# Optimization experiments

Measured on AMD Instinct MI355X. Metric: run time of the kernel, lower is better.

Reference implementation:

```python
import jax, jax.numpy as jnp
import numpy as np

B, SE, HD, ED, N, T = 64, 512, 1024, 512, 10000, 20
EOS_ID = 1
NEG_BIG = -1e9    # stand-in for -MAX_VAL encoder pad mask
MASK_VAL = -1e7   # logits_mask scatter value (-10000000.0 in torch)
M = HD + ED


def setup_inputs() -> dict:
    key = jax.random.key(0)
    ks = jax.random.split(key, 16)
    s = 0.02
    enc = jax.random.normal(ks[0], (B, SE, HD), jnp.float32)
    hidden = jax.random.normal(ks[1], (1, B, HD), jnp.float32)
    cell = jax.random.normal(ks[2], (1, B, HD), jnp.float32)
    text_lengths = jax.random.randint(ks[3], (B,), SE // 2, SE + 1)
    encoder_mask = jnp.arange(SE)[None, :] < text_lengths[:, None]  # [B,SE] bool
    embedding = jax.random.normal(ks[4], (N, ED), jnp.float32) * s
    # LSTM (PyTorch gate order i,f,g,o)
    w_ih = jax.random.normal(ks[5], (4 * HD, ED), jnp.float32) * s
    w_hh = jax.random.normal(ks[6], (4 * HD, HD), jnp.float32) * s
    b_ih = jnp.zeros((4 * HD,), jnp.float32)
    b_hh = jnp.zeros((4 * HD,), jnp.float32)
    # dense_net: Hd -> He
    w_q = jax.random.normal(ks[7], (HD, HD), jnp.float32) * s
    b_q = jnp.zeros((HD,), jnp.float32)
    # SelfAttentiveSum: Linear(Ed,Ed)+ReLU+Linear(Ed,1)
    w_k = jax.random.normal(ks[8], (ED, ED), jnp.float32) * s
    b_k = jnp.zeros((ED,), jnp.float32)
    w_ko = jax.random.normal(ks[9], (ED,), jnp.float32) * s
    b_ko = jnp.zeros((), jnp.float32)
    # MLP: Linear(M,M)+ReLU+Linear(M,N)
    w_m1 = jax.random.normal(ks[10], (M, M), jnp.float32) * s
    b_m1 = jnp.zeros((M,), jnp.float32)
    w_m2 = jax.random.normal(ks[11], (N, M), jnp.float32) * s
    b_m2 = jnp.zeros((N,), jnp.float32)
    return dict(encoded_hidden_embeddings=enc, hidden=hidden, cell=cell,
                text_lengths=text_lengths, encoder_mask=encoder_mask,
                embedding=embedding, w_ih=w_ih, w_hh=w_hh, b_ih=b_ih, b_hh=b_hh,
                w_q=w_q, b_q=b_q, w_k=w_k, b_k=b_k, w_ko=w_ko, b_ko=b_ko,
                w_m1=w_m1, b_m1=b_m1, w_m2=w_m2, b_m2=b_m2)


def _decode(enc, h0, c0, encoder_mask, embedding, w_ih, w_hh, b_ih, b_hh,
            w_q, b_q, w_k, b_k, w_ko, b_ko, w_m1, b_m1, w_m2, b_m2):
    pad_mask = jnp.where(encoder_mask, 0.0, NEG_BIG).astype(enc.dtype)  # [B,SE]
    sent = enc[:, 0, :]  # [B,HD] sentence representation (dropout is identity in eval)

    def step(carry, t):
        h, c, inp, logits_mask, buf = carry
        # --- LSTM cell (single step) ---
        gates = inp @ w_ih.T + b_ih + h @ w_hh.T + b_hh  # [B,4HD]
        i, f, g, o = jnp.split(gates, 4, axis=-1)
        c = jax.nn.sigmoid(f) * c + jax.nn.sigmoid(i) * jnp.tanh(g)
        h = jax.nn.sigmoid(o) * jnp.tanh(c)
        # --- attention over encoder states ---
        q = h @ w_q.T + b_q                                   # [B,HD]
        score = jnp.einsum('bsh,bh->bs', enc, q) + pad_mask    # [B,SE]
        w = jax.nn.softmax(score, axis=1)
        attn_enc = jnp.einsum('bs,bsh->bh', w, enc)            # [B,HD]
        # --- self-attentive sum over previously predicted label embeddings ---
        valid = jnp.arange(T) < jnp.maximum(t, 1)              # step 0: zeros row 0 valid
        k = jax.nn.relu(buf @ w_k.T + b_k) @ w_ko + b_ko       # [B,T]
        k = jnp.where(valid[None, :], k, NEG_BIG)
        sw = jax.nn.softmax(k, axis=1)
        attn_last = jnp.einsum('bt,bte->be', sw, buf)          # [B,ED]
        # --- MLP ---
        m = jnp.concatenate([sent + attn_enc, inp + attn_last], axis=-1)  # [B,M]
        logits = jax.nn.relu(m @ w_m1.T + b_m1) @ w_m2.T + b_m2 + logits_mask  # [B,N]
        next_ids = jnp.argmax(logits, axis=-1)                 # [B]
        pred_emb = embedding[next_ids]                          # [B,ED]
        buf = buf.at[:, t].set(pred_emb)
        logits_mask = logits_mask.at[jnp.arange(B), next_ids].set(MASK_VAL)
        logits_mask = logits_mask.at[:, EOS_ID].set(0.0)
        return (h, c, pred_emb, logits_mask, buf), (logits, next_ids)

    init = (h0, c0,
            jnp.zeros((B, ED), enc.dtype),
            jnp.zeros((B, N), enc.dtype),
            jnp.zeros((B, T, ED), enc.dtype))
    _, (outs, ids) = jax.lax.scan(step, init, jnp.arange(T))
    return jnp.transpose(outs, (1, 0, 2)), jnp.transpose(ids, (1, 0))  # [B,T,N],[B,T]


def reference(encoded_hidden_embeddings, hidden, cell, text_lengths, encoder_mask,
              embedding, w_ih, w_hh, b_ih, b_hh, w_q, b_q, w_k, b_k, w_ko, b_ko,
              w_m1, b_m1, w_m2, b_m2):
    # De=1: [1,B,HD] -> [B,HD]
    return _decode(encoded_hidden_embeddings, hidden[0], cell[0], encoder_mask,
                   embedding, w_ih, w_hh, b_ih, b_hh, w_q, b_q, w_k, b_k,
                   w_ko, b_ko, w_m1, b_m1, w_m2, b_m2)
```

## Files before the change

kernel.cpp:

```cpp
#include <hip/hip_runtime.h>

#define B64 64
#define SE 512
#define HD 1024
#define ED 512
#define NV 10000
#define TT 20
#define MM 1536
#define MASK_VALF -10000000.0f

#define OFF_XT    0
#define OFF_CT    98304
#define OFF_A     163840
#define OFF_B     4003840
#define OFF_QF    5052416
#define OFF_FM    5117952
#define OFF_FL    5118976
#define OFF_XT2   5120000
#define OFF_H1T   5218304
#define OFF_ARGV  5316608
#define OFF_ARGI  5396608
#define OFF_MASKT 5476608
#define OFF_BUF   6116608
#define OFF_BUFT  6771968
#define OFF_KVP   7427328

__device__ __forceinline__ float sigmoidf_(float x) { return 1.f / (1.f + expf(-x)); }

__global__ __launch_bounds__(256) void k_init(const float* __restrict__ h0,
                                              const float* __restrict__ c0,
                                              float* __restrict__ ws) {
  int idx = blockIdx.x * 256 + threadIdx.x, stride = gridDim.x * 256;
  float* inpT = ws + OFF_XT;
  float* hT = ws + OFF_XT + 512 * 64;
  float* cT = ws + OFF_CT;
  float* maskT = ws + OFF_MASKT;
  float* buf = ws + OFF_BUF;
  float* bufT = ws + OFF_BUFT;
  for (int i = idx; i < 512 * 64; i += stride) inpT[i] = 0.f;
  for (int i = idx; i < NV * 64; i += stride) maskT[i] = 0.f;
  for (int i = idx; i < B64 * TT * ED; i += stride) { buf[i] = 0.f; bufT[i] = 0.f; }
  for (int i = idx; i < HD * 64; i += stride) {
    int u = i >> 6, b = i & 63;
    hT[i] = h0[b * HD + u];
    cT[i] = c0[b * HD + u];
  }
}

template <int KT>
__global__ __launch_bounds__(256) void k_gemm(const float* __restrict__ W, int ldW,
                                              const float* __restrict__ x,
                                              float* __restrict__ part, int nrows, size_t psz) {
  __shared__ float wl[32][KT];
  int tid = threadIdx.x;
  int r0b = blockIdx.x * 32;
  int split = blockIdx.y;
  int k0 = split * KT;
  constexpr int NF4 = 32 * KT / 4;
  for (int i = tid; i < NF4; i += 256) {
    int r = i / (KT / 4), kk = (i % (KT / 4)) * 4;
    int gr = r0b + r;
    if (gr > nrows - 1) gr = nrows - 1;
    *(float4*)&wl[r][kk] = *(const float4*)&W[(size_t)gr * ldW + k0 + kk];
  }
  __syncthreads();
  int lane = tid & 63, wid = tid >> 6;
  const float* xp = x + (size_t)k0 * 64 + lane;
  float acc[8] = {0, 0, 0, 0, 0, 0, 0, 0};
#pragma unroll 2
  for (int k4 = 0; k4 < KT / 4; ++k4) {
    float x0 = xp[(4 * k4 + 0) * 64];
    float x1 = xp[(4 * k4 + 1) * 64];
    float x2 = xp[(4 * k4 + 2) * 64];
    float x3 = xp[(4 * k4 + 3) * 64];
#pragma unroll
    for (int i = 0; i < 8; ++i) {
      const float4 w4 = *(const float4*)&wl[wid * 8 + i][4 * k4];
      acc[i] = fmaf(w4.x, x0, acc[i]);
      acc[i] = fmaf(w4.y, x1, acc[i]);
      acc[i] = fmaf(w4.z, x2, acc[i]);
      acc[i] = fmaf(w4.w, x3, acc[i]);
    }
  }
  int r0 = r0b + wid * 8;
  float* o = part + (size_t)split * psz + (size_t)r0 * 64 + lane;
#pragma unroll
  for (int i = 0; i < 8; ++i)
    if (r0 + i < nrows) o[i * 64] = acc[i];
}

__global__ __launch_bounds__(256) void k_gates(const float* __restrict__ xt,
                                               const float* __restrict__ w_ih,
                                               const float* __restrict__ w_hh,
                                               float* __restrict__ gpart) {
  __shared__ float wl[32][256];
  int tid = threadIdx.x;
  int r0b = blockIdx.x * 32;
  int y = blockIdx.y;
  const float* W;
  int ldW, k0, xoff;
  if (y < 2) { W = w_ih; ldW = 512; k0 = y * 256; xoff = k0; }
  else { W = w_hh; ldW = 1024; k0 = (y - 2) * 256; xoff = 512 + k0; }
  for (int i = tid; i < 32 * 64; i += 256) {
    int r = i >> 6, kk = (i & 63) * 4;
    *(float4*)&wl[r][kk] = *(const float4*)&W[(size_t)(r0b + r) * ldW + k0 + kk];
  }
  __syncthreads();
  int lane = tid & 63, wid = tid >> 6;
  const float* xp = xt + (size_t)xoff * 64 + lane;
  float acc[8] = {0, 0, 0, 0, 0, 0, 0, 0};
#pragma unroll 2
  for (int k4 = 0; k4 < 64; ++k4) {
    float x0 = xp[(4 * k4 + 0) * 64];
    float x1 = xp[(4 * k4 + 1) * 64];
    float x2 = xp[(4 * k4 + 2) * 64];
    float x3 = xp[(4 * k4 + 3) * 64];
#pragma unroll
    for (int i = 0; i < 8; ++i) {
      const float4 w4 = *(const float4*)&wl[wid * 8 + i][4 * k4];
      acc[i] = fmaf(w4.x, x0, acc[i]);
      acc[i] = fmaf(w4.y, x1, acc[i]);
      acc[i] = fmaf(w4.z, x2, acc[i]);
      acc[i] = fmaf(w4.w, x3, acc[i]);
    }
  }
  int r0 = r0b + wid * 8;
  float* o = gpart + ((size_t)y * 262144 + (size_t)r0 * 64) + lane;
#pragma unroll
  for (int i = 0; i < 8; ++i) o[i * 64] = acc[i];
}

__global__ __launch_bounds__(256) void k_lstm(const float* __restrict__ gpart,
                                              const float* __restrict__ b_ih,
                                              const float* __restrict__ b_hh,
                                              float* __restrict__ cT, float* __restrict__ hT) {
  int i = blockIdx.x * 256 + threadIdx.x;
  int u = i >> 6, b = i & 63;
  float g4[4];
#pragma unroll
  for (int gi = 0; gi < 4; ++gi) {
    int r = gi * 1024 + u;
    float v = b_ih[r] + b_hh[r];
#pragma unroll
    for (int y = 0; y < 6; ++y) v += gpart[(size_t)y * 262144 + (size_t)r * 64 + b];
    g4[gi] = v;
  }
  float c = cT[i];
  float cn = sigmoidf_(g4[1]) * c + sigmoidf_(g4[0]) * tanhf(g4[2]);
  float hn = sigmoidf_(g4[3]) * tanhf(cn);
  cT[i] = cn;
  hT[i] = hn;
}

__global__ __launch_bounds__(256) void k_qfin(const float* __restrict__ qpart,
                                              const float* __restrict__ b_q,
                                              float* __restrict__ qf) {
  __shared__ float tile[64][65];
  int h0 = blockIdx.x * 64;
  int lane = threadIdx.x & 63, hrow = threadIdx.x >> 6;
#pragma unroll
  for (int p = 0; p < 16; ++p) {
    int hl = p * 4 + hrow;
    int h = h0 + hl;
    float v = b_q[h];
#pragma unroll
    for (int s = 0; s < 8; ++s) v += qpart[((size_t)s * 1024 + h) * 64 + lane];
    tile[hl][lane] = v;
  }
  __syncthreads();
#pragma unroll
  for (int p = 0; p < 16; ++p) {
    int b = p * 4 + hrow;
    qf[(size_t)b * 1024 + h0 + lane] = tile[lane][b];
  }
}

__global__ __launch_bounds__(256) void k_flash(const float* __restrict__ enc,
                                               const int* __restrict__ tlen,
                                               const float* __restrict__ qf,
                                               float* __restrict__ fm, float* __restrict__ fl,
                                               float* __restrict__ facc) {
  __shared__ float lacc[4][1024];
  __shared__ float lml[4][2];
  int b = blockIdx.x >> 4, split = blockIdx.x & 15;
  int tid = threadIdx.x, lane = tid & 63, wid = tid >> 6;
  int len = tlen[b];
  float qv[16];
#pragma unroll
  for (int j = 0; j < 4; ++j) {
    float4 tq = *(const float4*)&qf[(size_t)b * 1024 + j * 256 + lane * 4];
    qv[4 * j + 0] = tq.x; qv[4 * j + 1] = tq.y; qv[4 * j + 2] = tq.z; qv[4 * j + 3] = tq.w;
  }
  const float* base = enc + (size_t)b * SE * HD;
  int s0 = split * 32 + wid * 8;
  int nr = len - s0;
  nr = nr < 0 ? 0 : (nr > 8 ? 8 : nr);
  int npair = nr >> 1;

  float4 cA[4], cB[4], nA[4], nB[4];
  float m = -1e30f, l = 0.f, acc[16];
#pragma unroll
  for (int j = 0; j < 16; ++j) acc[j] = 0.f;

#define LOADROW(d, s)                                            \
  {                                                              \
    const float4* rp = (const float4*)(base + (size_t)(s)*HD) + lane; \
    d[0] = rp[0]; d[1] = rp[64]; d[2] = rp[128]; d[3] = rp[192]; \
  }

  if (npair > 0) { LOADROW(cA, s0); LOADROW(cB, s0 + 1); }
  for (int p = 0; p < npair; ++p) {
    if (p + 1 < npair) {
      LOADROW(nA, s0 + 2 * p + 2);
      LOADROW(nB, s0 + 2 * p + 3);
    } else if (nr & 1) {
      LOADROW(nA, s0 + nr - 1);
    }
    float d0 = 0.f, d1 = 0.f;
#pragma unroll
    for (int j = 0; j < 4; ++j) {
      d0 = fmaf(qv[4 * j + 0], cA[j].x, d0); d1 = fmaf(qv[4 * j + 0], cB[j].x, d1);
      d0 = fmaf(qv[4 * j + 1], cA[j].y, d0); d1 = fmaf(qv[4 * j + 1], cB[j].y, d1);
      d0 = fmaf(qv[4 * j + 2], cA[j].z, d0); d1 = fmaf(qv[4 * j + 2], cB[j].z, d1);
      d0 = fmaf(qv[4 * j + 3], cA[j].w, d0); d1 = fmaf(qv[4 * j + 3], cB[j].w, d1);
    }
#pragma unroll
    for (int off = 32; off; off >>= 1) { d0 += __shfl_xor(d0, off, 64); d1 += __shfl_xor(d1, off, 64); }
    d0 = __shfl(d0, 0, 64);
    d1 = __shfl(d1, 0, 64);
    float mn = fmaxf(m, fmaxf(d0, d1));
    float sc = expf(m - mn), p0 = expf(d0 - mn), p1 = expf(d1 - mn);
    l = l * sc + p0 + p1;
#pragma unroll
    for (int j = 0; j < 4; ++j) {
      acc[4 * j + 0] = fmaf(p1, cB[j].x, fmaf(p0, cA[j].x, acc[4 * j + 0] * sc));
      acc[4 * j + 1] = fmaf(p1, cB[j].y, fmaf(p0, cA[j].y, acc[4 * j + 1] * sc));
      acc[4 * j + 2] = fmaf(p1, cB[j].z, fmaf(p0, cA[j].z, acc[4 * j + 2] * sc));
      acc[4 * j + 3] = fmaf(p1, cB[j].w, fmaf(p0, cA[j].w, acc[4 * j + 3] * sc));
    }
    m = mn;
#pragma unroll
    for (int j = 0; j < 4; ++j) { cA[j] = nA[j]; cB[j] = nB[j]; }
  }
  if (nr & 1) {
    if (npair == 0) LOADROW(cA, s0);
    float d0 = 0.f;
#pragma unroll
    for (int j = 0; j < 4; ++j) {
      d0 = fmaf(qv[4 * j + 0], cA[j].x, d0);
      d0 = fmaf(qv[4 * j + 1], cA[j].y, d0);
      d0 = fmaf(qv[4 * j + 2], cA[j].z, d0);
      d0 = fmaf(qv[4 * j + 3], cA[j].w, d0);
    }
#pragma unroll
    for (int off = 32; off; off >>= 1) d0 += __shfl_xor(d0, off, 64);
    d0 = __shfl(d0, 0, 64);
    float mn = fmaxf(m, d0);
    float sc = expf(m - mn), p0 = expf(d0 - mn);
    l = l * sc + p0;
#pragma unroll
    for (int j = 0; j < 4; ++j) {
      acc[4 * j + 0] = fmaf(p0, cA[j].x, acc[4 * j + 0] * sc);
      acc[4 * j + 1] = fmaf(p0, cA[j].y, acc[4 * j + 1] * sc);
      acc[4 * j + 2] = fmaf(p0, cA[j].z, acc[4 * j + 2] * sc);
      acc[4 * j + 3] = fmaf(p0, cA[j].w, acc[4 * j + 3] * sc);
    }
    m = mn;
  }
#undef LOADROW
#pragma unroll
  for (int j = 0; j < 4; ++j)
    *(float4*)&lacc[wid][j * 256 + lane * 4] =
        make_float4(acc[4 * j], acc[4 * j + 1], acc[4 * j + 2], acc[4 * j + 3]);
  if (lane == 0) { lml[wid][0] = m; lml[wid][1] = l; }
  __syncthreads();
  float M = fmaxf(fmaxf(lml[0][0], lml[1][0]), fmaxf(lml[2][0], lml[3][0]));
  float w0 = expf(lml[0][0] - M), w1 = expf(lml[1][0] - M);
  float w2 = expf(lml[2][0] - M), w3 = expf(lml[3][0] - M);
  float L = w0 * lml[0][1] + w1 * lml[1][1] + w2 * lml[2][1] + w3 * lml[3][1];
  int p = b * 16 + split;
  for (int h = tid; h < 1024; h += 256)
    facc[(size_t)p * 1024 + h] =
        w0 * lacc[0][h] + w1 * lacc[1][h] + w2 * lacc[2][h] + w3 * lacc[3][h];
  if (tid == 0) { fm[p] = M; fl[p] = L; }
}

__global__ __launch_bounds__(256) void k_ctx(const float* __restrict__ enc,
                                             const float* __restrict__ fm,
                                             const float* __restrict__ fl,
                                             const float* __restrict__ facc,
                                             const float* __restrict__ kvp,
                                             const float* __restrict__ b_ko,
                                             const float* __restrict__ buf,
                                             const float* __restrict__ inpT,
                                             float* __restrict__ xT2, int tv) {
  __shared__ float pw[TT];
  int b = blockIdx.x, tid = threadIdx.x;
  if (tid < tv) {
    float s = b_ko[0];
    for (int g = 0; g < 64; ++g) s += kvp[((size_t)g * TT + tid) * 64 + b];
    pw[tid] = s;
  }
  __syncthreads();
  float mx = -1e30f;
  for (int k = 0; k < tv; ++k) mx = fmaxf(mx, pw[k]);
  float den = 0.f;
  for (int k = 0; k < tv; ++k) den += expf(pw[k] - mx);
  float invd = 1.f / den;
  __syncthreads();
  if (tid < tv) pw[tid] = expf(pw[tid] - mx) * invd;
  __syncthreads();
  float M = -1e30f;
#pragma unroll
  for (int k = 0; k < 16; ++k) M = fmaxf(M, fm[b * 16 + k]);
  float w[16];
  float L = 0.f;
#pragma unroll
  for (int k = 0; k < 16; ++k) {
    w[k] = expf(fm[b * 16 + k] - M);
    L += w[k] * fl[b * 16 + k];
  }
  float inv = 1.f / L;
  for (int h = tid; h < 1024; h += 256) {
    float s = 0.f;
#pragma unroll
    for (int k = 0; k < 16; ++k) s += w[k] * facc[(size_t)(b * 16 + k) * 1024 + h];
    xT2[h * 64 + b] = enc[(size_t)b * SE * HD + h] + s * inv;
  }
  for (int e = tid; e < 512; e += 256) {
    float a = 0.f;
    for (int k = 0; k < tv; ++k) a += pw[k] * buf[((size_t)b * TT + k) * 512 + e];
    xT2[(1024 + e) * 64 + b] = inpT[e * 64 + b] + a;
  }
}

__global__ __launch_bounds__(256) void k_kscore(const float* __restrict__ bufT,
                                                const float* __restrict__ w_k,
                                                const float* __restrict__ b_k,
                                                const float* __restrict__ w_ko,
                                                float* __restrict__ kvp, int j) {
  __shared__ float sacc[4][8][64];
  int lane = threadIdx.x & 63, wid = threadIdx.x >> 6;
  int ug = blockIdx.x;
  int u0 = ug * 8;
  int k0 = wid * 128;
  const float* xp = bufT + (size_t)j * 64 + lane;
  float acc[8] = {0, 0, 0, 0, 0, 0, 0, 0};
  for (int k4 = 0; k4 < 32; ++k4) {
    int e = k0 + 4 * k4;
    float x0 = xp[(size_t)(e + 0) * (TT * 64)];
    float x1 = xp[(size_t)(e + 1) * (TT * 64)];
    float x2 = xp[(size_t)(e + 2) * (TT * 64)];
    float x3 = xp[(size_t)(e + 3) * (TT * 64)];
#pragma unroll
    for (int i = 0; i < 8; ++i) {
      const float4 w4 = *(const float4*)&w_k[(size_t)(u0 + i) * 512 + e];
      acc[i] = fmaf(w4.x, x0, acc[i]);
      acc[i] = fmaf(w4.y, x1, acc[i]);
      acc[i] = fmaf(w4.z, x2, acc[i]);
      acc[i] = fmaf(w4.w, x3, acc[i]);
    }
  }
#pragma unroll
  for (int i = 0; i < 8; ++i) sacc[wid][i][lane] = acc[i];
  __syncthreads();
  if (wid == 0) {
    float kp = 0.f;
#pragma unroll
    for (int i = 0; i < 8; ++i) {
      float tot = b_k[u0 + i] + sacc[0][i][lane] + sacc[1][i][lane] + sacc[2][i][lane] +
                  sacc[3][i][lane];
      kp += fmaxf(tot, 0.f) * w_ko[u0 + i];
    }
    kvp[((size_t)ug * TT + j) * 64 + lane] = kp;
  }
}

__global__ __launch_bounds__(256) void k_h1comb(const float* __restrict__ h1part,
                                                const float* __restrict__ b_m1,
                                                float* __restrict__ h1T) {
  int i = blockIdx.x * 256 + threadIdx.x;
  int r = i >> 6;
  float v = b_m1[r];
#pragma unroll
  for (int s = 0; s < 12; ++s) v += h1part[(size_t)s * 98304 + i];
  h1T[i] = fmaxf(v, 0.f);
}

__global__ __launch_bounds__(256) void k_logfin(const float* __restrict__ lp,
                                                const float* __restrict__ b_m2,
                                                const float* __restrict__ maskT,
                                                float* __restrict__ argv, int* __restrict__ argi,
                                                float* __restrict__ out, int t) {
  __shared__ float tile[32][65];
  int lane = threadIdx.x & 63, wid = threadIdx.x >> 6;
  int rg = blockIdx.x * 4 + wid;
  int nb = blockIdx.x * 32;
  if (rg < 1250) {
    int r0 = rg * 8;
    float best = -3.4e38f;
    int bi = 0;
#pragma unroll
    for (int i = 0; i < 8; ++i) {
      int r = r0 + i;
      size_t idx = (size_t)r * 64 + lane;
      float v = b_m2[r] + maskT[idx];
#pragma unroll
      for (int s = 0; s < 6; ++s) v += lp[(size_t)s * 640000 + idx];
      tile[wid * 8 + i][lane] = v;
      if (v > best) { best = v; bi = r; }
    }
    argv[(size_t)rg * 64 + lane] = best;
    argi[(size_t)rg * 64 + lane] = bi;
  }
  __syncthreads();
  int b = threadIdx.x >> 2, q = threadIdx.x & 3;
  int nloc = q * 8;
  if (nb + nloc < NV) {
    float tmp[8];
#pragma unroll
    for (int c = 0; c < 8; ++c) tmp[c] = tile[nloc + c][b];
    float4* o = (float4*)&out[((size_t)b * TT + t) * NV + nb + nloc];
    o[0] = make_float4(tmp[0], tmp[1], tmp[2], tmp[3]);
    o[1] = make_float4(tmp[4], tmp[5], tmp[6], tmp[7]);
  }
}

__global__ __launch_bounds__(256) void k_final(const float* __restrict__ argv,
                                               const int* __restrict__ argi,
                                               const float* __restrict__ emb,
                                               float* __restrict__ maskT, float* __restrict__ inpT,
                                               float* __restrict__ buf, float* __restrict__ bufT,
                                               float* __restrict__ out_ids, int t) {
  __shared__ float sv[256];
  __shared__ int si_[256];
  __shared__ int sid;
  int b = blockIdx.x, tid = threadIdx.x;
  float best = -3.4e38f;
  int bi = 0x7fffffff;
  for (int g = tid; g < 1250; g += 256) {
    float v = argv[(size_t)g * 64 + b];
    int idx = argi[(size_t)g * 64 + b];
    if (v > best || (v == best && idx < bi)) { best = v; bi = idx; }
  }
  sv[tid] = best;
  si_[tid] = bi;
  __syncthreads();
  for (int off = 128; off; off >>= 1) {
    if (tid < off) {
      float v2 = sv[tid + off];
      int i2 = si_[tid + off];
      if (v2 > sv[tid] || (v2 == sv[tid] && i2 < si_[tid])) { sv[tid] = v2; si_[tid] = i2; }
    }
    __syncthreads();
  }
  if (tid == 0) {
    sid = si_[0];
    out_ids[b * TT + t] = (float)si_[0];
    if (si_[0] != 1) maskT[(size_t)si_[0] * 64 + b] = MASK_VALF;
  }
  __syncthreads();
  int id = sid;
  for (int e = tid; e < 512; e += 256) {
    float v = emb[(size_t)id * 512 + e];
    inpT[e * 64 + b] = v;
    buf[((size_t)b * TT + t) * 512 + e] = v;
    bufT[(size_t)e * (TT * 64) + t * 64 + b] = v;
  }
}

extern "C" void kernel_launch(void* const* d_in, const int* in_sizes, int n_in,
                              void* d_out, int out_size, void* d_ws, size_t ws_size,
                              hipStream_t stream) {
  const float* enc = (const float*)d_in[0];
  const float* h0 = (const float*)d_in[1];
  const float* c0 = (const float*)d_in[2];
  const int* tlen = (const int*)d_in[3];
  const float* emb = (const float*)d_in[5];
  const float* w_ih = (const float*)d_in[6];
  const float* w_hh = (const float*)d_in[7];
  const float* b_ih = (const float*)d_in[8];
  const float* b_hh = (const float*)d_in[9];
  const float* w_q = (const float*)d_in[10];
  const float* b_q = (const float*)d_in[11];
  const float* w_k = (const float*)d_in[12];
  const float* b_k = (const float*)d_in[13];
  const float* w_ko = (const float*)d_in[14];
  const float* b_ko = (const float*)d_in[15];
  const float* w_m1 = (const float*)d_in[16];
  const float* b_m1 = (const float*)d_in[17];
  const float* w_m2 = (const float*)d_in[18];
  const float* b_m2 = (const float*)d_in[19];

  float* ws = (float*)d_ws;
  float* out_logits = (float*)d_out;
  float* out_ids = out_logits + (size_t)B64 * TT * NV;

  float* xt = ws + OFF_XT;
  float* hT = xt + 512 * 64;

  k_init<<<2048, 256, 0, stream>>>(h0, c0, ws);
  k_kscore<<<64, 256, 0, stream>>>(ws + OFF_BUFT, w_k, b_k, w_ko, ws + OFF_KVP, 0);

  for (int t = 0; t < TT; ++t) {
    int tv = (t < 1) ? 1 : t;
    k_gates<<<dim3(128, 6), 256, 0, stream>>>(xt, w_ih, w_hh, ws + OFF_A);
    k_lstm<<<256, 256, 0, stream>>>(ws + OFF_A, b_ih, b_hh, ws + OFF_CT, hT);
    k_gemm<128><<<dim3(32, 8), 256, 0, stream>>>(w_q, 1024, hT, ws + OFF_B, 1024, 65536);
    k_qfin<<<16, 256, 0, stream>>>(ws + OFF_B, b_q, ws + OFF_QF);
    k_flash<<<1024, 256, 0, stream>>>(enc, tlen, ws + OFF_QF, ws + OFF_FM, ws + OFF_FL,
                                      ws + OFF_B);
    k_ctx<<<64, 256, 0, stream>>>(enc, ws + OFF_FM, ws + OFF_FL, ws + OFF_B, ws + OFF_KVP, b_ko,
                                  ws + OFF_BUF, xt, ws + OFF_XT2, tv);
    k_gemm<128><<<dim3(48, 12), 256, 0, stream>>>(w_m1, MM, ws + OFF_XT2, ws + OFF_A, MM, 98304);
    k_h1comb<<<384, 256, 0, stream>>>(ws + OFF_A, b_m1, ws + OFF_H1T);
    k_gemm<256><<<dim3(313, 6), 256, 0, stream>>>(w_m2, MM, ws + OFF_H1T, ws + OFF_A, NV, 640000);
    k_logfin<<<313, 256, 0, stream>>>(ws + OFF_A, b_m2, ws + OFF_MASKT, ws + OFF_ARGV,
                                      (int*)(ws + OFF_ARGI), out_logits, t);
    k_final<<<64, 256, 0, stream>>>(ws + OFF_ARGV, (int*)(ws + OFF_ARGI), emb, ws + OFF_MASKT, xt,
                                    ws + OFF_BUF, ws + OFF_BUFT, out_ids, t);
    if (t < TT - 1)
      k_kscore<<<64, 256, 0, stream>>>(ws + OFF_BUFT, w_k, b_k, w_ko, ws + OFF_KVP, t);
  }
}
```

Measured before the change: 3.328 ms.

## Fuse split-K GEMMs with their reductions and double-buffer the LSTM state

Each per-step split-K GEMM now reduces its partial sums in shared memory and applies the epilogue in the same kernel. This covers LSTM gates plus cell update, the query projection, the MLP first layer with ReLU, and the output layer with mask, row argmax and logit store. The separate combine kernels and their partial-sum round trips through global memory go away. Input and hidden state are ping-ponged between two buffers so the fused cell kernel can write h without racing its readers, and the context kernel is split across four blocks per batch row. The fused kernels use fewer, larger blocks with 48KB of shared memory each, which may lower occupancy. The logits store now writes 8 scattered floats per row instead of coalesced float4s.

```diff
diff --git a/kernel.cpp b/kernel.cpp
--- a/kernel.cpp
+++ b/kernel.cpp
@@ -9,21 +9,21 @@
 #define MM 1536
 #define MASK_VALF -10000000.0f
 
-#define OFF_XT    0
-#define OFF_CT    98304
-#define OFF_A     163840
-#define OFF_B     4003840
-#define OFF_QF    5052416
-#define OFF_FM    5117952
-#define OFF_FL    5118976
-#define OFF_XT2   5120000
-#define OFF_H1T   5218304
-#define OFF_ARGV  5316608
-#define OFF_ARGI  5396608
-#define OFF_MASKT 5476608
-#define OFF_BUF   6116608
-#define OFF_BUFT  6771968
-#define OFF_KVP   7427328
+#define OFF_XA    0
+#define OFF_XB    98304
+#define OFF_CT    196608
+#define OFF_QF    262144
+#define OFF_FM    327680
+#define OFF_FL    328704
+#define OFF_FACC  329728
+#define OFF_XT2   1378304
+#define OFF_H1T   1476608
+#define OFF_ARGV  1574912
+#define OFF_ARGI  1654912
+#define OFF_MASKT 1734912
+#define OFF_BUF   2374912
+#define OFF_BUFT  3030272
+#define OFF_KVP   3685632
 
 __device__ __forceinline__ float sigmoidf_(float x) { return 1.f / (1.f + expf(-x)); }
 
@@ -31,83 +31,100 @@
                                               const float* __restrict__ c0,
                                               float* __restrict__ ws) {
   int idx = blockIdx.x * 256 + threadIdx.x, stride = gridDim.x * 256;
-  float* inpT = ws + OFF_XT;
-  float* hT = ws + OFF_XT + 512 * 64;
+  float* xa = ws + OFF_XA;
   float* cT = ws + OFF_CT;
   float* maskT = ws + OFF_MASKT;
   float* buf = ws + OFF_BUF;
   float* bufT = ws + OFF_BUFT;
-  for (int i = idx; i < 512 * 64; i += stride) inpT[i] = 0.f;
+  for (int i = idx; i < 512 * 64; i += stride) xa[i] = 0.f;
   for (int i = idx; i < NV * 64; i += stride) maskT[i] = 0.f;
   for (int i = idx; i < B64 * TT * ED; i += stride) { buf[i] = 0.f; bufT[i] = 0.f; }
   for (int i = idx; i < HD * 64; i += stride) {
     int u = i >> 6, b = i & 63;
-    hT[i] = h0[b * HD + u];
+    xa[512 * 64 + i] = h0[b * HD + u];
     cT[i] = c0[b * HD + u];
   }
 }
 
-template <int KT>
-__global__ __launch_bounds__(256) void k_gemm(const float* __restrict__ W, int ldW,
-                                              const float* __restrict__ x,
-                                              float* __restrict__ part, int nrows, size_t psz) {
-  __shared__ float wl[32][KT];
+__global__ __launch_bounds__(256) void k_cell(const float* __restrict__ xcur,
+                                              const float* __restrict__ w_ih,
+                                              const float* __restrict__ w_hh,
+                                              const float* __restrict__ b_ih,
+                                              const float* __restrict__ b_hh,
+                                              float* __restrict__ cT,
+                                              float* __restrict__ xnext) {
+  __shared__ float wl[8 * 1536];
   int tid = threadIdx.x;
-  int r0b = blockIdx.x * 32;
-  int split = blockIdx.y;
-  int k0 = split * KT;
-  constexpr int NF4 = 32 * KT / 4;
-  for (int i = tid; i < NF4; i += 256) {
-    int r = i / (KT / 4), kk = (i % (KT / 4)) * 4;
-    int gr = r0b + r;
-    if (gr > nrows - 1) gr = nrows - 1;
-    *(float4*)&wl[r][kk] = *(const float4*)&W[(size_t)gr * ldW + k0 + kk];
+  int u0 = blockIdx.x * 2;
+  for (int i = tid; i < 3072; i += 256) {
+    int lr = i / 384, kq = i % 384;
+    int k = kq * 4;
+    int grow = (lr >> 1) * 1024 + u0 + (lr & 1);
+    float4 v;
+    if (k < 512) v = *(const float4*)&w_ih[(size_t)grow * 512 + k];
+    else v = *(const float4*)&w_hh[(size_t)grow * 1024 + (k - 512)];
+    *(float4*)&wl[lr * 1536 + k] = v;
   }
   __syncthreads();
   int lane = tid & 63, wid = tid >> 6;
-  const float* xp = x + (size_t)k0 * 64 + lane;
+  int kbase = wid * 384;
+  const float* xp = xcur + (size_t)kbase * 64 + lane;
   float acc[8] = {0, 0, 0, 0, 0, 0, 0, 0};
 #pragma unroll 2
-  for (int k4 = 0; k4 < KT / 4; ++k4) {
+  for (int k4 = 0; k4 < 96; ++k4) {
     float x0 = xp[(4 * k4 + 0) * 64];
     float x1 = xp[(4 * k4 + 1) * 64];
     float x2 = xp[(4 * k4 + 2) * 64];
     float x3 = xp[(4 * k4 + 3) * 64];
 #pragma unroll
-    for (int i = 0; i < 8; ++i) {
-      const float4 w4 = *(const float4*)&wl[wid * 8 + i][4 * k4];
-      acc[i] = fmaf(w4.x, x0, acc[i]);
-      acc[i] = fmaf(w4.y, x1, acc[i]);
-      acc[i] = fmaf(w4.z, x2, acc[i]);
-      acc[i] = fmaf(w4.w, x3, acc[i]);
-    }
-  }
-  int r0 = r0b + wid * 8;
-  float* o = part + (size_t)split * psz + (size_t)r0 * 64 + lane;
-#pragma unroll
-  for (int i = 0; i < 8; ++i)
-    if (r0 + i < nrows) o[i * 64] = acc[i];
-}
-
-__global__ __launch_bounds__(256) void k_gates(const float* __restrict__ xt,
-                                               const float* __restrict__ w_ih,
-                                               const float* __restrict__ w_hh,
-                                               float* __restrict__ gpart) {
-  __shared__ float wl[32][256];
+    for (int lr = 0; lr < 8; ++lr) {
+      const float4 w4 = *(const float4*)&wl[lr * 1536 + kbase + 4 * k4];
+      acc[lr] = fmaf(w4.x, x0, acc[lr]);
+      acc[lr] = fmaf(w4.y, x1, acc[lr]);
+      acc[lr] = fmaf(w4.z, x2, acc[lr]);
+      acc[lr] = fmaf(w4.w, x3, acc[lr]);
+    }
+  }
+  __syncthreads();
+#pragma unroll
+  for (int lr = 0; lr < 8; ++lr) wl[wid * 512 + lr * 64 + lane] = acc[lr];
+  __syncthreads();
+  if (tid < 128) {
+    int j = tid >> 6, b = tid & 63;
+    float g4[4];
+#pragma unroll
+    for (int g = 0; g < 4; ++g) {
+      int lr = g * 2 + j;
+      int grow = g * 1024 + u0 + j;
+      float v = b_ih[grow] + b_hh[grow];
+#pragma unroll
+      for (int w = 0; w < 4; ++w) v += wl[w * 512 + lr * 64 + b];
+      g4[g] = v;
+    }
+    int u = u0 + j;
+    float c = cT[u * 64 + b];
+    float cn = sigmoidf_(g4[1]) * c + sigmoidf_(g4[0]) * tanhf(g4[2]);
+    float hn = sigmoidf_(g4[3]) * tanhf(cn);
+    cT[u * 64 + b] = cn;
+    xnext[(512 + u) * 64 + b] = hn;
+  }
+}
+
+__global__ __launch_bounds__(256) void k_q2(const float* __restrict__ h,
+                                            const float* __restrict__ w_q,
+                                            const float* __restrict__ b_q,
+                                            float* __restrict__ qf) {
+  __shared__ float wl[8 * 1024];
   int tid = threadIdx.x;
-  int r0b = blockIdx.x * 32;
-  int y = blockIdx.y;
-  const float* W;
-  int ldW, k0, xoff;
-  if (y < 2) { W = w_ih; ldW = 512; k0 = y * 256; xoff = k0; }
-  else { W = w_hh; ldW = 1024; k0 = (y - 2) * 256; xoff = 512 + k0; }
-  for (int i = tid; i < 32 * 64; i += 256) {
-    int r = i >> 6, kk = (i & 63) * 4;
-    *(float4*)&wl[r][kk] = *(const float4*)&W[(size_t)(r0b + r) * ldW + k0 + kk];
+  int h0 = blockIdx.x * 8;
+  for (int i = tid; i < 2048; i += 256) {
+    int lr = i >> 8, kq = i & 255;
+    *(float4*)&wl[lr * 1024 + kq * 4] = *(const float4*)&w_q[(size_t)(h0 + lr) * 1024 + kq * 4];
   }
   __syncthreads();
   int lane = tid & 63, wid = tid >> 6;
-  const float* xp = xt + (size_t)xoff * 64 + lane;
+  int kbase = wid * 256;
+  const float* xp = h + (size_t)kbase * 64 + lane;
   float acc[8] = {0, 0, 0, 0, 0, 0, 0, 0};
 #pragma unroll 2
   for (int k4 = 0; k4 < 64; ++k4) {
@@ -116,62 +133,24 @@
     float x2 = xp[(4 * k4 + 2) * 64];
     float x3 = xp[(4 * k4 + 3) * 64];
 #pragma unroll
-    for (int i = 0; i < 8; ++i) {
-      const float4 w4 = *(const float4*)&wl[wid * 8 + i][4 * k4];
-      acc[i] = fmaf(w4.x, x0, acc[i]);
-      acc[i] = fmaf(w4.y, x1, acc[i]);
-      acc[i] = fmaf(w4.z, x2, acc[i]);
-      acc[i] = fmaf(w4.w, x3, acc[i]);
-    }
-  }
-  int r0 = r0b + wid * 8;
-  float* o = gpart + ((size_t)y * 262144 + (size_t)r0 * 64) + lane;
-#pragma unroll
-  for (int i = 0; i < 8; ++i) o[i * 64] = acc[i];
-}
-
-__global__ __launch_bounds__(256) void k_lstm(const float* __restrict__ gpart,
-                                              const float* __restrict__ b_ih,
-                                              const float* __restrict__ b_hh,
-                                              float* __restrict__ cT, float* __restrict__ hT) {
-  int i = blockIdx.x * 256 + threadIdx.x;
-  int u = i >> 6, b = i & 63;
-  float g4[4];
-#pragma unroll
-  for (int gi = 0; gi < 4; ++gi) {
-    int r = gi * 1024 + u;
-    float v = b_ih[r] + b_hh[r];
-#pragma unroll
-    for (int y = 0; y < 6; ++y) v += gpart[(size_t)y * 262144 + (size_t)r * 64 + b];
-    g4[gi] = v;
-  }
-  float c = cT[i];
-  float cn = sigmoidf_(g4[1]) * c + sigmoidf_(g4[0]) * tanhf(g4[2]);
-  float hn = sigmoidf_(g4[3]) * tanhf(cn);
-  cT[i] = cn;
-  hT[i] = hn;
-}
-
-__global__ __launch_bounds__(256) void k_qfin(const float* __restrict__ qpart,
-                                              const float* __restrict__ b_q,
-                                              float* __restrict__ qf) {
-  __shared__ float tile[64][65];
-  int h0 = blockIdx.x * 64;
-  int lane = threadIdx.x & 63, hrow = threadIdx.x >> 6;
-#pragma unroll
-  for (int p = 0; p < 16; ++p) {
-    int hl = p * 4 + hrow;
-    int h = h0 + hl;
-    float v = b_q[h];
-#pragma unroll
-    for (int s = 0; s < 8; ++s) v += qpart[((size_t)s * 1024 + h) * 64 + lane];
-    tile[hl][lane] = v;
-  }
-  __syncthreads();
-#pragma unroll
-  for (int p = 0; p < 16; ++p) {
-    int b = p * 4 + hrow;
-    qf[(size_t)b * 1024 + h0 + lane] = tile[lane][b];
+    for (int lr = 0; lr < 8; ++lr) {
+      const float4 w4 = *(const float4*)&wl[lr * 1024 + kbase + 4 * k4];
+      acc[lr] = fmaf(w4.x, x0, acc[lr]);
+      acc[lr] = fmaf(w4.y, x1, acc[lr]);
+      acc[lr] = fmaf(w4.z, x2, acc[lr]);
+      acc[lr] = fmaf(w4.w, x3, acc[lr]);
+    }
+  }
+  __syncthreads();
+#pragma unroll
+  for (int lr = 0; lr < 8; ++lr) wl[wid * 512 + lr * 64 + lane] = acc[lr];
+  __syncthreads();
+  for (int e = tid; e < 512; e += 256) {
+    int lr = e >> 6, b = e & 63;
+    float v = b_q[h0 + lr];
+#pragma unroll
+    for (int w = 0; w < 4; ++w) v += wl[w * 512 + lr * 64 + b];
+    qf[(size_t)b * 1024 + h0 + lr] = v;
   }
 }
 
@@ -202,10 +181,10 @@
 #pragma unroll
   for (int j = 0; j < 16; ++j) acc[j] = 0.f;
 
-#define LOADROW(d, s)                                            \
-  {                                                              \
+#define LOADROW(d, s)                                                 \
+  {                                                                   \
     const float4* rp = (const float4*)(base + (size_t)(s)*HD) + lane; \
-    d[0] = rp[0]; d[1] = rp[64]; d[2] = rp[128]; d[3] = rp[192]; \
+    d[0] = rp[0]; d[1] = rp[64]; d[2] = rp[128]; d[3] = rp[192];      \
   }
 
   if (npair > 0) { LOADROW(cA, s0); LOADROW(cB, s0 + 1); }
@@ -295,7 +274,8 @@
                                              const float* __restrict__ inpT,
                                              float* __restrict__ xT2, int tv) {
   __shared__ float pw[TT];
-  int b = blockIdx.x, tid = threadIdx.x;
+  int b = blockIdx.x >> 2, qd = blockIdx.x & 3;
+  int tid = threadIdx.x;
   if (tid < tv) {
     float s = b_ko[0];
     for (int g = 0; g < 64; ++g) s += kvp[((size_t)g * TT + tid) * 64 + b];
@@ -321,16 +301,170 @@
     L += w[k] * fl[b * 16 + k];
   }
   float inv = 1.f / L;
-  for (int h = tid; h < 1024; h += 256) {
+  {
+    int h = qd * 256 + tid;
     float s = 0.f;
 #pragma unroll
     for (int k = 0; k < 16; ++k) s += w[k] * facc[(size_t)(b * 16 + k) * 1024 + h];
     xT2[h * 64 + b] = enc[(size_t)b * SE * HD + h] + s * inv;
   }
-  for (int e = tid; e < 512; e += 256) {
+  if (tid < 128) {
+    int e = qd * 128 + tid;
     float a = 0.f;
     for (int k = 0; k < tv; ++k) a += pw[k] * buf[((size_t)b * TT + k) * 512 + e];
     xT2[(1024 + e) * 64 + b] = inpT[e * 64 + b] + a;
+  }
+}
+
+__global__ __launch_bounds__(256) void k_h12(const float* __restrict__ xT2,
+                                             const float* __restrict__ w_m1,
+                                             const float* __restrict__ b_m1,
+                                             float* __restrict__ h1T) {
+  __shared__ float wl[8 * 1536];
+  int tid = threadIdx.x;
+  int r0 = blockIdx.x * 8;
+  for (int i = tid; i < 3072; i += 256) {
+    int lr = i / 384, kq = i % 384;
+    *(float4*)&wl[lr * 1536 + kq * 4] = *(const float4*)&w_m1[(size_t)(r0 + lr) * MM + kq * 4];
+  }
+  __syncthreads();
+  int lane = tid & 63, wid = tid >> 6;
+  int kbase = wid * 384;
+  const float* xp = xT2 + (size_t)kbase * 64 + lane;
+  float acc[8] = {0, 0, 0, 0, 0, 0, 0, 0};
+#pragma unroll 2
+  for (int k4 = 0; k4 < 96; ++k4) {
+    float x0 = xp[(4 * k4 + 0) * 64];
+    float x1 = xp[(4 * k4 + 1) * 64];
+    float x2 = xp[(4 * k4 + 2) * 64];
+    float x3 = xp[(4 * k4 + 3) * 64];
+#pragma unroll
+    for (int lr = 0; lr < 8; ++lr) {
+      const float4 w4 = *(const float4*)&wl[lr * 1536 + kbase + 4 * k4];
+      acc[lr] = fmaf(w4.x, x0, acc[lr]);
+      acc[lr] = fmaf(w4.y, x1, acc[lr]);
+      acc[lr] = fmaf(w4.z, x2, acc[lr]);
+      acc[lr] = fmaf(w4.w, x3, acc[lr]);
+    }
+  }
+  __syncthreads();
+#pragma unroll
+  for (int lr = 0; lr < 8; ++lr) wl[wid * 512 + lr * 64 + lane] = acc[lr];
+  __syncthreads();
+  for (int e = tid; e < 512; e += 256) {
+    int lr = e >> 6, b = e & 63;
+    float v = b_m1[r0 + lr];
+#pragma unroll
+    for (int w = 0; w < 4; ++w) v += wl[w * 512 + lr * 64 + b];
+    h1T[(size_t)(r0 + lr) * 64 + b] = fmaxf(v, 0.f);
+  }
+}
+
+__global__ __launch_bounds__(256) void k_glogfin2(const float* __restrict__ h1T,
+                                                  const float* __restrict__ w_m2,
+                                                  const float* __restrict__ b_m2,
+                                                  const float* __restrict__ maskT,
+                                                  float* __restrict__ argv, int* __restrict__ argi,
+                                                  float* __restrict__ out, int t) {
+  __shared__ float wl[8 * 1536];
+  int tid = threadIdx.x;
+  int r0 = blockIdx.x * 8;
+  for (int i = tid; i < 3072; i += 256) {
+    int lr = i / 384, kq = i % 384;
+    *(float4*)&wl[lr * 1536 + kq * 4] = *(const float4*)&w_m2[(size_t)(r0 + lr) * MM + kq * 4];
+  }
+  __syncthreads();
+  int lane = tid & 63, wid = tid >> 6;
+  int kbase = wid * 384;
+  const float* xp = h1T + (size_t)kbase * 64 + lane;
+  float acc[8] = {0, 0, 0, 0, 0, 0, 0, 0};
+#pragma unroll 2
+  for (int k4 = 0; k4 < 96; ++k4) {
+    float x0 = xp[(4 * k4 + 0) * 64];
+    float x1 = xp[(4 * k4 + 1) * 64];
+    float x2 = xp[(4 * k4 + 2) * 64];
+    float x3 = xp[(4 * k4 + 3) * 64];
+#pragma unroll
+    for (int lr = 0; lr < 8; ++lr) {
+      const float4 w4 = *(const float4*)&wl[lr * 1536 + kbase + 4 * k4];
+      acc[lr] = fmaf(w4.x, x0, acc[lr]);
+      acc[lr] = fmaf(w4.y, x1, acc[lr]);
+      acc[lr] = fmaf(w4.z, x2, acc[lr]);
+      acc[lr] = fmaf(w4.w, x3, acc[lr]);
+    }
+  }
+  __syncthreads();
+#pragma unroll
+  for (int lr = 0; lr < 8; ++lr) wl[wid * 512 + lr * 64 + lane] = acc[lr];
+  __syncthreads();
+  for (int e = tid; e < 512; e += 256) {
+    int lr = e >> 6, b = e & 63;
+    int r = r0 + lr;
+    float v = b_m2[r] + maskT[(size_t)r * 64 + b];
+#pragma unroll
+    for (int w = 0; w < 4; ++w) v += wl[w * 512 + lr * 64 + b];
+    wl[2048 + lr * 64 + b] = v;
+  }
+  __syncthreads();
+  if (tid < 64) {
+    int b = tid;
+    float best = -3.4e38f;
+    int bi = 0;
+#pragma unroll
+    for (int lr = 0; lr < 8; ++lr) {
+      float v = wl[2048 + lr * 64 + b];
+      if (v > best) { best = v; bi = r0 + lr; }
+    }
+    argv[(size_t)blockIdx.x * 64 + b] = best;
+    argi[(size_t)blockIdx.x * 64 + b] = bi;
+  }
+  for (int e = tid; e < 512; e += 256) {
+    int b = e >> 3, lr = e & 7;
+    out[((size_t)b * TT + t) * NV + r0 + lr] = wl[2048 + lr * 64 + b];
+  }
+}
+
+__global__ __launch_bounds__(256) void k_final(const float* __restrict__ argv,
+                                               const int* __restrict__ argi,
+                                               const float* __restrict__ emb,
+                                               float* __restrict__ maskT,
+                                               float* __restrict__ xnext,
+                                               float* __restrict__ buf, float* __restrict__ bufT,
+                                               float* __restrict__ out_ids, int t) {
+  __shared__ float sv[256];
+  __shared__ int si_[256];
+  __shared__ int sid;
+  int b = blockIdx.x, tid = threadIdx.x;
+  float best = -3.4e38f;
+  int bi = 0x7fffffff;
+  for (int g = tid; g < 1250; g += 256) {
+    float v = argv[(size_t)g * 64 + b];
+    int idx = argi[(size_t)g * 64 + b];
+    if (v > best || (v == best && idx < bi)) { best = v; bi = idx; }
+  }
+  sv[tid] = best;
+  si_[tid] = bi;
+  __syncthreads();
+  for (int off = 128; off; off >>= 1) {
+    if (tid < off) {
+      float v2 = sv[tid + off];
+      int i2 = si_[tid + off];
+      if (v2 > sv[tid] || (v2 == sv[tid] && i2 < si_[tid])) { sv[tid] = v2; si_[tid] = i2; }
+    }
+    __syncthreads();
+  }
+  if (tid == 0) {
+    sid = si_[0];
+    out_ids[b * TT + t] = (float)si_[0];
+    if (si_[0] != 1) maskT[(size_t)si_[0] * 64 + b] = MASK_VALF;
+  }
+  __syncthreads();
+  int id = sid;
+  for (int e = tid; e < 512; e += 256) {
+    float v = emb[(size_t)id * 512 + e];
+    xnext[e * 64 + b] = v;
+    buf[((size_t)b * TT + t) * 512 + e] = v;
+    bufT[(size_t)e * (TT * 64) + t * 64 + b] = v;
   }
 }
 
@@ -373,99 +507,6 @@
       kp += fmaxf(tot, 0.f) * w_ko[u0 + i];
     }
     kvp[((size_t)ug * TT + j) * 64 + lane] = kp;
-  }
-}
-
-__global__ __launch_bounds__(256) void k_h1comb(const float* __restrict__ h1part,
-                                                const float* __restrict__ b_m1,
-                                                float* __restrict__ h1T) {
-  int i = blockIdx.x * 256 + threadIdx.x;
-  int r = i >> 6;
-  float v = b_m1[r];
-#pragma unroll
-  for (int s = 0; s < 12; ++s) v += h1part[(size_t)s * 98304 + i];
-  h1T[i] = fmaxf(v, 0.f);
-}
-
-__global__ __launch_bounds__(256) void k_logfin(const float* __restrict__ lp,
-                                                const float* __restrict__ b_m2,
-                                                const float* __restrict__ maskT,
-                                                float* __restrict__ argv, int* __restrict__ argi,
-                                                float* __restrict__ out, int t) {
-  __shared__ float tile[32][65];
-  int lane = threadIdx.x & 63, wid = threadIdx.x >> 6;
-  int rg = blockIdx.x * 4 + wid;
-  int nb = blockIdx.x * 32;
-  if (rg < 1250) {
-    int r0 = rg * 8;
-    float best = -3.4e38f;
-    int bi = 0;
-#pragma unroll
-    for (int i = 0; i < 8; ++i) {
-      int r = r0 + i;
-      size_t idx = (size_t)r * 64 + lane;
-      float v = b_m2[r] + maskT[idx];
-#pragma unroll
-      for (int s = 0; s < 6; ++s) v += lp[(size_t)s * 640000 + idx];
-      tile[wid * 8 + i][lane] = v;
-      if (v > best) { best = v; bi = r; }
-    }
-    argv[(size_t)rg * 64 + lane] = best;
-    argi[(size_t)rg * 64 + lane] = bi;
-  }
-  __syncthreads();
-  int b = threadIdx.x >> 2, q = threadIdx.x & 3;
-  int nloc = q * 8;
-  if (nb + nloc < NV) {
-    float tmp[8];
-#pragma unroll
-    for (int c = 0; c < 8; ++c) tmp[c] = tile[nloc + c][b];
-    float4* o = (float4*)&out[((size_t)b * TT + t) * NV + nb + nloc];
-    o[0] = make_float4(tmp[0], tmp[1], tmp[2], tmp[3]);
-    o[1] = make_float4(tmp[4], tmp[5], tmp[6], tmp[7]);
-  }
-}
-
-__global__ __launch_bounds__(256) void k_final(const float* __restrict__ argv,
-                                               const int* __restrict__ argi,
-                                               const float* __restrict__ emb,
-                                               float* __restrict__ maskT, float* __restrict__ inpT,
-                                               float* __restrict__ buf, float* __restrict__ bufT,
-                                               float* __restrict__ out_ids, int t) {
-  __shared__ float sv[256];
-  __shared__ int si_[256];
-  __shared__ int sid;
-  int b = blockIdx.x, tid = threadIdx.x;
-  float best = -3.4e38f;
-  int bi = 0x7fffffff;
-  for (int g = tid; g < 1250; g += 256) {
-    float v = argv[(size_t)g * 64 + b];
-    int idx = argi[(size_t)g * 64 + b];
-    if (v > best || (v == best && idx < bi)) { best = v; bi = idx; }
-  }
-  sv[tid] = best;
-  si_[tid] = bi;
-  __syncthreads();
-  for (int off = 128; off; off >>= 1) {
-    if (tid < off) {
-      float v2 = sv[tid + off];
-      int i2 = si_[tid + off];
-      if (v2 > sv[tid] || (v2 == sv[tid] && i2 < si_[tid])) { sv[tid] = v2; si_[tid] = i2; }
-    }
-    __syncthreads();
-  }
-  if (tid == 0) {
-    sid = si_[0];
-    out_ids[b * TT + t] = (float)si_[0];
-    if (si_[0] != 1) maskT[(size_t)si_[0] * 64 + b] = MASK_VALF;
-  }
-  __syncthreads();
-  int id = sid;
-  for (int e = tid; e < 512; e += 256) {
-    float v = emb[(size_t)id * 512 + e];
-    inpT[e * 64 + b] = v;
-    buf[((size_t)b * TT + t) * 512 + e] = v;
-    bufT[(size_t)e * (TT * 64) + t * 64 + b] = v;
   }
 }
 
@@ -496,29 +537,24 @@
   float* out_logits = (float*)d_out;
   float* out_ids = out_logits + (size_t)B64 * TT * NV;
 
-  float* xt = ws + OFF_XT;
-  float* hT = xt + 512 * 64;
-
   k_init<<<2048, 256, 0, stream>>>(h0, c0, ws);
   k_kscore<<<64, 256, 0, stream>>>(ws + OFF_BUFT, w_k, b_k, w_ko, ws + OFF_KVP, 0);
 
   for (int t = 0; t < TT; ++t) {
     int tv = (t < 1) ? 1 : t;
-    k_gates<<<dim3(128, 6), 256, 0, stream>>>(xt, w_ih, w_hh, ws + OFF_A);
-    k_lstm<<<256, 256, 0, stream>>>(ws + OFF_A, b_ih, b_hh, ws + OFF_CT, hT);
-    k_gemm<128><<<dim3(32, 8), 256, 0, stream>>>(w_q, 1024, hT, ws + OFF_B, 1024, 65536);
-    k_qfin<<<16, 256, 0, stream>>>(ws + OFF_B, b_q, ws + OFF_QF);
+    float* xcur = ws + ((t & 1) ? OFF_XB : OFF_XA);
+    float* xnext = ws + ((t & 1) ? OFF_XA : OFF_XB);
+    k_cell<<<512, 256, 0, stream>>>(xcur, w_ih, w_hh, b_ih, b_hh, ws + OFF_CT, xnext);
+    k_q2<<<128, 256, 0, stream>>>(xnext + 512 * 64, w_q, b_q, ws + OFF_QF);
     k_flash<<<1024, 256, 0, stream>>>(enc, tlen, ws + OFF_QF, ws + OFF_FM, ws + OFF_FL,
-                                      ws + OFF_B);
-    k_ctx<<<64, 256, 0, stream>>>(enc, ws + OFF_FM, ws + OFF_FL, ws + OFF_B, ws + OFF_KVP, b_ko,
-                                  ws + OFF_BUF, xt, ws + OFF_XT2, tv);
-    k_gemm<128><<<dim3(48, 12), 256, 0, stream>>>(w_m1, MM, ws + OFF_XT2, ws + OFF_A, MM, 98304);
-    k_h1comb<<<384, 256, 0, stream>>>(ws + OFF_A, b_m1, ws + OFF_H1T);
-    k_gemm<256><<<dim3(313, 6), 256, 0, stream>>>(w_m2, MM, ws + OFF_H1T, ws + OFF_A, NV, 640000);
-    k_logfin<<<313, 256, 0, stream>>>(ws + OFF_A, b_m2, ws + OFF_MASKT, ws + OFF_ARGV,
-                                      (int*)(ws + OFF_ARGI), out_logits, t);
-    k_final<<<64, 256, 0, stream>>>(ws + OFF_ARGV, (int*)(ws + OFF_ARGI), emb, ws + OFF_MASKT, xt,
-                                    ws + OFF_BUF, ws + OFF_BUFT, out_ids, t);
+                                      ws + OFF_FACC);
+    k_ctx<<<256, 256, 0, stream>>>(enc, ws + OFF_FM, ws + OFF_FL, ws + OFF_FACC, ws + OFF_KVP,
+                                   b_ko, ws + OFF_BUF, xcur, ws + OFF_XT2, tv);
+    k_h12<<<192, 256, 0, stream>>>(ws + OFF_XT2, w_m1, b_m1, ws + OFF_H1T);
+    k_glogfin2<<<1250, 256, 0, stream>>>(ws + OFF_H1T, w_m2, b_m2, ws + OFF_MASKT, ws + OFF_ARGV,
+                                         (int*)(ws + OFF_ARGI), out_logits, t);
+    k_final<<<64, 256, 0, stream>>>(ws + OFF_ARGV, (int*)(ws + OFF_ARGI), emb, ws + OFF_MASKT,
+                                    xnext, ws + OFF_BUF, ws + OFF_BUFT, out_ids, t);
     if (t < TT - 1)
       k_kscore<<<64, 256, 0, stream>>>(ws + OFF_BUFT, w_k, b_k, w_ko, ws + OFF_KVP, t);
   }
```

Result: slower. 3.491 ms (+4.9%).
